# Optimization experiments

Hardware: AMD Instinct MI355X
Metric: run time of the kernel (lower is better)

## Reference

```python
import jax, jax.numpy as jnp
import numpy as np

B = 1024
IN_Q = 2048
IN_KV = 2048
NH = 16
D = 64
INNER = NH * D
TF = 4
NC = 2
EPS = 1e-5
SLOPE = 0.01  # LeakyReLU default negative slope


def setup_inputs() -> dict:
    key = jax.random.key(0)
    ks = jax.random.split(key, 8)
    s = 0.02
    return {
        "q_input": jax.random.normal(ks[0], (B, IN_Q), jnp.float32),
        "kv_input": jax.random.normal(ks[1], (B, IN_KV), jnp.float32),
        "Wq": jax.random.normal(ks[2], (INNER, IN_Q), jnp.float32) * s,
        "bq": jax.random.normal(ks[3], (INNER,), jnp.float32) * s,
        "Wkv": jax.random.normal(ks[4], (2 * INNER, IN_KV), jnp.float32) * s,
        "bkv": jax.random.normal(ks[5], (2 * INNER,), jnp.float32) * s,
        "bn_w": jnp.ones((TF,), jnp.float32),
        "bn_b": jnp.zeros((TF,), jnp.float32),
        "Wo": jax.random.normal(ks[6], (NC, TF), jnp.float32) * s,
        "bo": jax.random.normal(ks[7], (NC,), jnp.float32) * s,
    }


def reference(q_input, kv_input, Wq, bq, Wkv, bkv, bn_w, bn_b, Wo, bo):
    b = q_input.shape[0]
    # projections: [B, NH, D] and [B, NH, 2D]
    q = (q_input @ Wq.T + bq).reshape(b, NH, D)
    kv = (kv_input @ Wkv.T + bkv).reshape(b, NH, 2 * D)
    k, v = kv[..., :D], kv[..., D:]
    # sim[b,n] = k[b,n,:] . q[b,n,:]  (per-head scalar score)
    sim = jnp.einsum("bnd,bnd->bn", k, q)
    att = jax.nn.softmax(sim, axis=-1)  # softmax over heads
    # torch.matmul([B,NH], [B,NH,D]) broadcast -> out[i,j,:] = sum_n att[j,n] v[i,n,:]
    att_out = jnp.einsum("jn,ind->ijd", att, v)  # [B, B, D]
    flat = att_out.reshape(b, b * D)  # [B, B*D]
    # AdaptiveAvgPool1d to TF bins (L % TF == 0 -> exact reshape-mean)
    pooled = flat.reshape(b, TF, (b * D) // TF).mean(axis=-1)  # [B, TF]
    x = jnp.where(pooled >= 0, pooled, SLOPE * pooled)  # LeakyReLU
    # BatchNorm1d, train mode (batch stats, biased variance)
    mean = x.mean(axis=0)
    var = x.var(axis=0)
    x = (x - mean) * jax.lax.rsqrt(var + EPS) * bn_w + bn_b
    # dropout(p=0.0) is identity
    return x @ Wo.T + bo  # [B, NC]
```

## Files before the change

kernel.cpp:

```cpp
#include <hip/hip_runtime.h>
#include <hip/hip_bf16.h>

#define EPS 1e-5f
#define SLOPE 0.01f

typedef __attribute__((ext_vector_type(8))) short bfrag8;
typedef __attribute__((ext_vector_type(4))) float f32x4;

#define AS1 __attribute__((address_space(1)))
#define AS3 __attribute__((address_space(3)))

#define WS_SIM_OFF   0u
#define WS_S_OFF     65536u
#define WS_WVS_OFF   131072u
#define WS_BVS_OFF   262144u
#define WS_OUT_OFF   262208u
#define WS_AIMG_OFF  8650816u
#define WS_BIMG_OFF  25428032u

__device__ __forceinline__ unsigned short f2bf(float f) {
    union { float f; unsigned int u; } x; x.f = f;
    unsigned int r = (x.u + 0x7FFFu + ((x.u >> 16) & 1u)) >> 16;
    return (unsigned short)r;
}
__device__ __forceinline__ uint4 pack8(const float4& a, const float4& b) {
    uint4 r;
    r.x = (unsigned)f2bf(a.x) | ((unsigned)f2bf(a.y) << 16);
    r.y = (unsigned)f2bf(a.z) | ((unsigned)f2bf(a.w) << 16);
    r.z = (unsigned)f2bf(b.x) | ((unsigned)f2bf(b.y) << 16);
    r.w = (unsigned)f2bf(b.z) | ((unsigned)f2bf(b.w) << 16);
    return r;
}

#define PREP_A    524288
#define PREP_B2   (PREP_A + 524288)
#define PREP_WVSE (PREP_B2 + 32768)
#define PREP_END  (PREP_WVSE + 16)

__global__ __launch_bounds__(256) void prep_kernel(
        const float* __restrict__ qin, const float* __restrict__ kvin,
        const float* __restrict__ Wq, const float* __restrict__ Wkv,
        const float* __restrict__ bkv, unsigned char* __restrict__ ws) {
    int gid = blockIdx.x * 256 + threadIdx.x;
    if (gid < PREP_A) {
        int p  = gid & 511;
        int kt = (gid >> 9) & 31;
        int mt = (gid >> 14) & 15;
        int s2 = gid >> 18;
        int rit = p >> 3;
        int gk = (p & 7) ^ (rit & 7);
        int row = mt * 64 + rit;
        int k = kt * 64 + gk * 8;
        const float* src = (s2 ? kvin : qin) + (size_t)row * 2048 + k;
        float4 v0 = *(const float4*)src;
        float4 v1 = *(const float4*)(src + 4);
        *(uint4*)(ws + WS_AIMG_OFF + (size_t)gid * 16) = pack8(v0, v1);
    } else if (gid < PREP_B2) {
        int g2 = gid - PREP_A;
        int p  = g2 & 511;
        int kt = (g2 >> 9) & 31;
        int nt = g2 >> 14;
        int cit = p >> 3;
        int gk = (p & 7) ^ (cit & 7);
        int col = nt * 64 + cit;
        int k = kt * 64 + gk * 8;
        const float* wrow;
        if (col < 1024) wrow = Wq + (size_t)col * 2048;
        else {
            int c2 = col - 1024;
            wrow = Wkv + (size_t)(((c2 >> 6) << 7) + (c2 & 63)) * 2048;
        }
        float4 v0 = *(const float4*)(wrow + k);
        float4 v1 = *(const float4*)(wrow + k + 4);
        *(uint4*)(ws + WS_BIMG_OFF + (size_t)g2 * 16) = pack8(v0, v1);
    } else if (gid < PREP_WVSE) {
        int g2 = gid - PREP_B2;
        int n = g2 >> 11, c = g2 & 2047;
        const float* base = Wkv + (size_t)(n * 128 + 64) * 2048 + c;
        float s = 0.f;
        #pragma unroll 8
        for (int d = 0; d < 64; ++d) s += base[(size_t)d * 2048];
        ((float*)(ws + WS_WVS_OFF))[c * 16 + n] = s;
    } else if (gid < PREP_END) {
        int n = gid - PREP_WVSE;
        float b = 0.f;
        #pragma unroll
        for (int d = 0; d < 64; ++d) b += bkv[n * 128 + 64 + d];
        ((float*)(ws + WS_BVS_OFF))[n] = b;
    }
}

__global__ __launch_bounds__(256) void gemm_qk_kernel(unsigned char* __restrict__ ws) {
    __shared__ alignas(16) unsigned short LA[2][4096];
    __shared__ alignas(16) unsigned short LB[2][4096];

    const int t = threadIdx.x;
    const int w = t >> 6, l = t & 63;
    const int nt = blockIdx.x, mt = blockIdx.y;
    const int wr = w >> 1, wc = w & 1;
    const int lrow = l & 15, lhi = l >> 4;

    const unsigned char* aBase = ws + WS_AIMG_OFF
        + (size_t)((nt >= 16) ? 4194304u : 0u) + (size_t)mt * 262144u;
    const unsigned char* bBase = ws + WS_BIMG_OFF + (size_t)nt * 262144u;
    float* Out = (float*)(ws + WS_OUT_OFF);

    int offA[2][2], offB[2][2];
    #pragma unroll
    for (int ks = 0; ks < 2; ++ks)
        #pragma unroll
        for (int i = 0; i < 2; ++i) {
            int rA = wr * 32 + i * 16 + lrow;
            int rB = wc * 32 + i * 16 + lrow;
            offA[ks][i] = rA * 128 + (((ks * 4 + lhi) ^ (rA & 7)) << 4);
            offB[ks][i] = rB * 128 + (((ks * 4 + lhi) ^ (rB & 7)) << 4);
        }

    f32x4 acc00 = (f32x4)0.f, acc01 = (f32x4)0.f, acc10 = (f32x4)0.f, acc11 = (f32x4)0.f;

#define STAGE(kt_, buf_) do {                                                        \
    const unsigned char* _as = aBase + (size_t)(kt_) * 8192;                         \
    const unsigned char* _bs = bBase + (size_t)(kt_) * 8192;                         \
    unsigned char* _ad = ((unsigned char*)&LA[0][0]) + (buf_) * 8192;                \
    unsigned char* _bd = ((unsigned char*)&LB[0][0]) + (buf_) * 8192;                \
    _Pragma("unroll")                                                                \
    for (int _j = 0; _j < 2; ++_j) {                                                 \
        int _p = _j * 256 + t;                                                       \
        __builtin_amdgcn_global_load_lds(                                            \
            (const AS1 unsigned int*)(const void*)(_as + _p * 16),                   \
            (AS3 unsigned int*)(void*)(_ad + _p * 16), 16, 0, 0);                    \
        __builtin_amdgcn_global_load_lds(                                            \
            (const AS1 unsigned int*)(const void*)(_bs + _p * 16),                   \
            (AS3 unsigned int*)(void*)(_bd + _p * 16), 16, 0, 0);                    \
    } } while (0)

    STAGE(0, 0);
    __syncthreads();

    for (int kt = 0; kt < 32; ++kt) {
        const int cur = kt & 1;
        if (kt < 31) STAGE(kt + 1, cur ^ 1);
        const char* la = (const char*)&LA[0][0] + cur * 8192;
        const char* lb = (const char*)&LB[0][0] + cur * 8192;
        bfrag8 fa00 = *(const bfrag8*)(la + offA[0][0]);
        bfrag8 fa01 = *(const bfrag8*)(la + offA[0][1]);
        bfrag8 fa10 = *(const bfrag8*)(la + offA[1][0]);
        bfrag8 fa11 = *(const bfrag8*)(la + offA[1][1]);
        bfrag8 fb00 = *(const bfrag8*)(lb + offB[0][0]);
        bfrag8 fb01 = *(const bfrag8*)(lb + offB[0][1]);
        bfrag8 fb10 = *(const bfrag8*)(lb + offB[1][0]);
        bfrag8 fb11 = *(const bfrag8*)(lb + offB[1][1]);
        acc00 = __builtin_amdgcn_mfma_f32_16x16x32_bf16(fa00, fb00, acc00, 0, 0, 0);
        acc01 = __builtin_amdgcn_mfma_f32_16x16x32_bf16(fa00, fb01, acc01, 0, 0, 0);
        acc10 = __builtin_amdgcn_mfma_f32_16x16x32_bf16(fa01, fb00, acc10, 0, 0, 0);
        acc11 = __builtin_amdgcn_mfma_f32_16x16x32_bf16(fa01, fb01, acc11, 0, 0, 0);
        acc00 = __builtin_amdgcn_mfma_f32_16x16x32_bf16(fa10, fb10, acc00, 0, 0, 0);
        acc01 = __builtin_amdgcn_mfma_f32_16x16x32_bf16(fa10, fb11, acc01, 0, 0, 0);
        acc10 = __builtin_amdgcn_mfma_f32_16x16x32_bf16(fa11, fb10, acc10, 0, 0, 0);
        acc11 = __builtin_amdgcn_mfma_f32_16x16x32_bf16(fa11, fb11, acc11, 0, 0, 0);
        __syncthreads();
    }
#undef STAGE

    f32x4 acc[2][2] = {{acc00, acc01}, {acc10, acc11}};
    #pragma unroll
    for (int mi = 0; mi < 2; ++mi)
        #pragma unroll
        for (int ni = 0; ni < 2; ++ni) {
            int col = nt * 64 + wc * 32 + ni * 16 + lrow;
            #pragma unroll
            for (int r = 0; r < 4; ++r) {
                int row = mt * 64 + wr * 32 + mi * 16 + lhi * 4 + r;
                Out[(size_t)row * 2048 + col] = acc[mi][ni][r];
            }
        }
}

__global__ __launch_bounds__(256) void sim_kernel(
        const float* __restrict__ bq, const float* __restrict__ bkv,
        unsigned char* __restrict__ ws) {
    int b = blockIdx.x, t = threadIdx.x;
    int w = t >> 6, d = t & 63;
    const float* orow = (const float*)(ws + WS_OUT_OFF) + (size_t)b * 2048;
    float* sim = (float*)(ws + WS_SIM_OFF);
    #pragma unroll
    for (int hh = 0; hh < 4; ++hh) {
        int h = w * 4 + hh;
        float qv = orow[h * 64 + d]        + bq[h * 64 + d];
        float kv = orow[1024 + h * 64 + d] + bkv[h * 128 + d];
        float p = qv * kv;
        p += __shfl_xor(p, 1);  p += __shfl_xor(p, 2);
        p += __shfl_xor(p, 4);  p += __shfl_xor(p, 8);
        p += __shfl_xor(p, 16); p += __shfl_xor(p, 32);
        if (d == 0) sim[b * 16 + h] = p;
    }
}

__global__ __launch_bounds__(256) void s_kernel(
        const float* __restrict__ kvin, unsigned char* __restrict__ ws) {
    int b = blockIdx.x, t = threadIdx.x;
    int w = t >> 6, l = t & 63;
    __shared__ float SW[4][16];
    int n = t & 15, g = t >> 4;
    const float* kvrow = kvin + (size_t)b * 2048;
    const float* wv = (const float*)(ws + WS_WVS_OFF);
    float p = 0.f;
    #pragma unroll 4
    for (int tt = 0; tt < 128; ++tt) {
        int c = g + (tt << 4);
        p = fmaf(kvrow[c], wv[c * 16 + n], p);
    }
    p += __shfl_xor(p, 16);
    p += __shfl_xor(p, 32);
    if (l < 16) SW[w][n] = p;
    __syncthreads();
    if (t < 16) {
        float sv = SW[0][t] + SW[1][t] + SW[2][t] + SW[3][t]
                 + ((const float*)(ws + WS_BVS_OFF))[t];
        ((float*)(ws + WS_S_OFF))[b * 16 + t] = sv;
    }
}

__global__ __launch_bounds__(1024) void final_kernel(
        const float* __restrict__ bn_w, const float* __restrict__ bn_b,
        const float* __restrict__ Wo, const float* __restrict__ bo,
        const unsigned char* __restrict__ ws, float* __restrict__ out) {
    int t = threadIdx.x;
    int w = t >> 6;
    int l = t & 63;
    __shared__ float Aw[16][16];
    __shared__ float Af[4][16];
    __shared__ float SWs[16][8];
    __shared__ float FS[8];
    __shared__ float sc[4], sh[4];

    float a16[16];
    {
        const float* srow = (const float*)(ws + WS_SIM_OFF) + (size_t)t * 16;
        float4 v0 = *(const float4*)(srow + 0);
        float4 v1 = *(const float4*)(srow + 4);
        float4 v2 = *(const float4*)(srow + 8);
        float4 v3 = *(const float4*)(srow + 12);
        a16[0]=v0.x; a16[1]=v0.y; a16[2]=v0.z; a16[3]=v0.w;
        a16[4]=v1.x; a16[5]=v1.y; a16[6]=v1.z; a16[7]=v1.w;
        a16[8]=v2.x; a16[9]=v2.y; a16[10]=v2.z; a16[11]=v2.w;
        a16[12]=v3.x; a16[13]=v3.y; a16[14]=v3.z; a16[15]=v3.w;
        float m = a16[0];
        #pragma unroll
        for (int n = 1; n < 16; ++n) m = fmaxf(m, a16[n]);
        float den = 0.f;
        #pragma unroll
        for (int n = 0; n < 16; ++n) { a16[n] = expf(a16[n] - m); den += a16[n]; }
        float inv = 1.f / den;
        #pragma unroll
        for (int n = 0; n < 16; ++n) a16[n] *= inv;
    }
    #pragma unroll
    for (int n = 0; n < 16; ++n) {
        float p = a16[n];
        p += __shfl_xor(p, 1);  p += __shfl_xor(p, 2);
        p += __shfl_xor(p, 4);  p += __shfl_xor(p, 8);
        p += __shfl_xor(p, 16); p += __shfl_xor(p, 32);
        a16[n] = p;
    }
    if (l == 0) {
        #pragma unroll
        for (int n = 0; n < 16; ++n) Aw[w][n] = a16[n];
    }
    __syncthreads();
    if (t < 64) {
        int f = t >> 4, n = t & 15;
        Af[f][n] = Aw[4*f][n] + Aw[4*f+1][n] + Aw[4*f+2][n] + Aw[4*f+3][n];
    }
    __syncthreads();

    float sv[16];
    {
        const float* srow = (const float*)(ws + WS_S_OFF) + (size_t)t * 16;
        float4 v0 = *(const float4*)(srow + 0);
        float4 v1 = *(const float4*)(srow + 4);
        float4 v2 = *(const float4*)(srow + 8);
        float4 v3 = *(const float4*)(srow + 12);
        sv[0]=v0.x; sv[1]=v0.y; sv[2]=v0.z; sv[3]=v0.w;
        sv[4]=v1.x; sv[5]=v1.y; sv[6]=v1.z; sv[7]=v1.w;
        sv[8]=v2.x; sv[9]=v2.y; sv[10]=v2.z; sv[11]=v2.w;
        sv[12]=v3.x; sv[13]=v3.y; sv[14]=v3.z; sv[15]=v3.w;
    }
    float x[4];
    #pragma unroll
    for (int f = 0; f < 4; ++f) {
        float p = 0.f;
        #pragma unroll
        for (int n = 0; n < 16; ++n) p = fmaf(Af[f][n], sv[n], p);
        p *= (1.f / 16384.f);
        x[f] = (p >= 0.f) ? p : SLOPE * p;
    }

    float st[8];
    #pragma unroll
    for (int f = 0; f < 4; ++f) { st[f] = x[f]; st[4 + f] = x[f] * x[f]; }
    #pragma unroll
    for (int j = 0; j < 8; ++j) {
        float p = st[j];
        p += __shfl_xor(p, 1);  p += __shfl_xor(p, 2);
        p += __shfl_xor(p, 4);  p += __shfl_xor(p, 8);
        p += __shfl_xor(p, 16); p += __shfl_xor(p, 32);
        st[j] = p;
    }
    if (l == 0) {
        #pragma unroll
        for (int j = 0; j < 8; ++j) SWs[w][j] = st[j];
    }
    __syncthreads();
    if (t < 8) {
        float p = 0.f;
        #pragma unroll
        for (int ww = 0; ww < 16; ++ww) p += SWs[ww][t];
        FS[t] = p;
    }
    __syncthreads();
    if (t < 4) {
        float mean = FS[t] * (1.f / 1024.f);
        float var  = FS[4 + t] * (1.f / 1024.f) - mean * mean;
        float s = bn_w[t] / sqrtf(var + EPS);
        sc[t] = s;
        sh[t] = bn_b[t] - mean * s;
    }
    __syncthreads();

    float o0 = bo[0], o1 = bo[1];
    #pragma unroll
    for (int f = 0; f < 4; ++f) {
        float xh = x[f] * sc[f] + sh[f];
        o0 = fmaf(xh, Wo[f], o0);
        o1 = fmaf(xh, Wo[4 + f], o1);
    }
    *(float2*)(out + (size_t)t * 2) = make_float2(o0, o1);
}

extern "C" void kernel_launch(void* const* d_in, const int* in_sizes, int n_in,
                              void* d_out, int out_size, void* d_ws, size_t ws_size,
                              hipStream_t stream) {
    const float* q_input  = (const float*)d_in[0];
    const float* kv_input = (const float*)d_in[1];
    const float* Wq   = (const float*)d_in[2];
    const float* bq   = (const float*)d_in[3];
    const float* Wkv  = (const float*)d_in[4];
    const float* bkv  = (const float*)d_in[5];
    const float* bn_w = (const float*)d_in[6];
    const float* bn_b = (const float*)d_in[7];
    const float* Wo   = (const float*)d_in[8];
    const float* bo   = (const float*)d_in[9];
    float* out = (float*)d_out;
    unsigned char* ws = (unsigned char*)d_ws;

    hipLaunchKernelGGL(prep_kernel, dim3((PREP_END + 255) / 256), dim3(256), 0, stream,
                       q_input, kv_input, Wq, Wkv, bkv, ws);
    hipLaunchKernelGGL(gemm_qk_kernel, dim3(32, 16), dim3(256), 0, stream, ws);
    hipLaunchKernelGGL(sim_kernel, dim3(1024), dim3(256), 0, stream, bq, bkv, ws);
    hipLaunchKernelGGL(s_kernel, dim3(1024), dim3(256), 0, stream, kv_input, ws);
    hipLaunchKernelGGL(final_kernel, dim3(1), dim3(1024), 0, stream,
                       bn_w, bn_b, Wo, bo, ws, out);
}
```

Measured before the change: 72.43 us.

## Triple-buffer GEMM K-loop with async LDS loads and merge sim/s kernels

The QK GEMM moves from double to triple buffering. Loads are issued two tiles ahead, and explicit vmcnt waits plus raw s_barrier replace the __syncthreads, so global-to-LDS transfers overlap more MFMA work and each iteration needs only one barrier. The sim and s kernels are merged into a single launch, removing one kernel launch and its gap. LDS use per block grows to 48KB, which may limit occupancy, and the hand-written waitcnt logic carries a correctness risk.

```diff
diff --git a/kernel.cpp b/kernel.cpp
--- a/kernel.cpp
+++ b/kernel.cpp
@@ -90,9 +90,9 @@
     }
 }
 
-__global__ __launch_bounds__(256) void gemm_qk_kernel(unsigned char* __restrict__ ws) {
-    __shared__ alignas(16) unsigned short LA[2][4096];
-    __shared__ alignas(16) unsigned short LB[2][4096];
+__global__ __launch_bounds__(256, 2) void gemm_qk_kernel(unsigned char* __restrict__ ws) {
+    __shared__ alignas(16) unsigned short LA[3][4096];
+    __shared__ alignas(16) unsigned short LB[3][4096];
 
     const int t = threadIdx.x;
     const int w = t >> 6, l = t & 63;
@@ -121,8 +121,8 @@
 #define STAGE(kt_, buf_) do {                                                        \
     const unsigned char* _as = aBase + (size_t)(kt_) * 8192;                         \
     const unsigned char* _bs = bBase + (size_t)(kt_) * 8192;                         \
-    unsigned char* _ad = ((unsigned char*)&LA[0][0]) + (buf_) * 8192;                \
-    unsigned char* _bd = ((unsigned char*)&LB[0][0]) + (buf_) * 8192;                \
+    unsigned char* _ad = ((unsigned char*)&LA[0][0]) + (size_t)(buf_) * 8192;        \
+    unsigned char* _bd = ((unsigned char*)&LB[0][0]) + (size_t)(buf_) * 8192;        \
     _Pragma("unroll")                                                                \
     for (int _j = 0; _j < 2; ++_j) {                                                 \
         int _p = _j * 256 + t;                                                       \
@@ -135,11 +135,14 @@
     } } while (0)
 
     STAGE(0, 0);
-    __syncthreads();
-
+    STAGE(1, 1);
+    asm volatile("s_waitcnt vmcnt(4)" ::: "memory");
+    __builtin_amdgcn_sched_barrier(0);
+    __builtin_amdgcn_s_barrier();
+    __builtin_amdgcn_sched_barrier(0);
+
+    int cur = 0, nxt = 2;
     for (int kt = 0; kt < 32; ++kt) {
-        const int cur = kt & 1;
-        if (kt < 31) STAGE(kt + 1, cur ^ 1);
         const char* la = (const char*)&LA[0][0] + cur * 8192;
         const char* lb = (const char*)&LB[0][0] + cur * 8192;
         bfrag8 fa00 = *(const bfrag8*)(la + offA[0][0]);
@@ -158,7 +161,17 @@
         acc01 = __builtin_amdgcn_mfma_f32_16x16x32_bf16(fa10, fb11, acc01, 0, 0, 0);
         acc10 = __builtin_amdgcn_mfma_f32_16x16x32_bf16(fa11, fb10, acc10, 0, 0, 0);
         acc11 = __builtin_amdgcn_mfma_f32_16x16x32_bf16(fa11, fb11, acc11, 0, 0, 0);
-        __syncthreads();
+        if (kt < 30) {
+            STAGE(kt + 2, nxt);
+            asm volatile("s_waitcnt vmcnt(4)" ::: "memory");
+        } else {
+            asm volatile("s_waitcnt vmcnt(0)" ::: "memory");
+        }
+        __builtin_amdgcn_sched_barrier(0);
+        __builtin_amdgcn_s_barrier();
+        __builtin_amdgcn_sched_barrier(0);
+        cur = (cur == 2) ? 0 : cur + 1;
+        nxt = (nxt == 2) ? 0 : nxt + 1;
     }
 #undef STAGE
 
@@ -176,30 +189,26 @@
         }
 }
 
-__global__ __launch_bounds__(256) void sim_kernel(
+__global__ __launch_bounds__(256) void sim_s_kernel(
         const float* __restrict__ bq, const float* __restrict__ bkv,
-        unsigned char* __restrict__ ws) {
-    int b = blockIdx.x, t = threadIdx.x;
-    int w = t >> 6, d = t & 63;
-    const float* orow = (const float*)(ws + WS_OUT_OFF) + (size_t)b * 2048;
-    float* sim = (float*)(ws + WS_SIM_OFF);
-    #pragma unroll
-    for (int hh = 0; hh < 4; ++hh) {
-        int h = w * 4 + hh;
-        float qv = orow[h * 64 + d]        + bq[h * 64 + d];
-        float kv = orow[1024 + h * 64 + d] + bkv[h * 128 + d];
-        float p = qv * kv;
-        p += __shfl_xor(p, 1);  p += __shfl_xor(p, 2);
-        p += __shfl_xor(p, 4);  p += __shfl_xor(p, 8);
-        p += __shfl_xor(p, 16); p += __shfl_xor(p, 32);
-        if (d == 0) sim[b * 16 + h] = p;
-    }
-}
-
-__global__ __launch_bounds__(256) void s_kernel(
         const float* __restrict__ kvin, unsigned char* __restrict__ ws) {
     int b = blockIdx.x, t = threadIdx.x;
     int w = t >> 6, l = t & 63;
+    {
+        const float* orow = (const float*)(ws + WS_OUT_OFF) + (size_t)b * 2048;
+        float* sim = (float*)(ws + WS_SIM_OFF);
+        #pragma unroll
+        for (int hh = 0; hh < 4; ++hh) {
+            int h = w * 4 + hh;
+            float qv = orow[h * 64 + l]        + bq[h * 64 + l];
+            float kv = orow[1024 + h * 64 + l] + bkv[h * 128 + l];
+            float p = qv * kv;
+            p += __shfl_xor(p, 1);  p += __shfl_xor(p, 2);
+            p += __shfl_xor(p, 4);  p += __shfl_xor(p, 8);
+            p += __shfl_xor(p, 16); p += __shfl_xor(p, 32);
+            if (l == 0) sim[b * 16 + h] = p;
+        }
+    }
     __shared__ float SW[4][16];
     int n = t & 15, g = t >> 4;
     const float* kvrow = kvin + (size_t)b * 2048;
@@ -357,8 +366,8 @@
     hipLaunchKernelGGL(prep_kernel, dim3((PREP_END + 255) / 256), dim3(256), 0, stream,
                        q_input, kv_input, Wq, Wkv, bkv, ws);
     hipLaunchKernelGGL(gemm_qk_kernel, dim3(32, 16), dim3(256), 0, stream, ws);
-    hipLaunchKernelGGL(sim_kernel, dim3(1024), dim3(256), 0, stream, bq, bkv, ws);
-    hipLaunchKernelGGL(s_kernel, dim3(1024), dim3(256), 0, stream, kv_input, ws);
+    hipLaunchKernelGGL(sim_s_kernel, dim3(1024), dim3(256), 0, stream,
+                       bq, bkv, kv_input, ws);
     hipLaunchKernelGGL(final_kernel, dim3(1), dim3(1024), 0, stream,
                        bn_w, bn_b, Wo, bo, ws, out);
 }
```

Measured after the change: 62.94 us. -13.1%, faster.
